# Kernel tuning notes

Measured on AMD Instinct MI355X. Metric: run time of the kernel, lower is better.

Reference implementation:

```python
import jax, jax.numpy as jnp
import numpy as np

N_NODES = 50000
N_EDGES = 800000
IN_CH = 64
OUT_CH = 64
HEADS = 4
NEG_SLOPE = 0.2  # PyG GATConv default


def setup_inputs() -> dict:
    key = jax.random.key(0)
    ks = jax.random.split(key, 8)
    x = jax.random.normal(ks[0], (N_NODES, IN_CH), dtype=jnp.float32)
    edge_index = jax.random.randint(ks[1], (2, N_EDGES), 0, N_NODES, dtype=jnp.int64)
    # GATConv params (concat=False): lin weight [in, H*out], att vectors [H, out], bias [out]
    W = jax.random.normal(ks[2], (IN_CH, HEADS * OUT_CH), dtype=jnp.float32) * (1.0 / np.sqrt(IN_CH))
    att_src = jax.random.normal(ks[3], (HEADS, OUT_CH), dtype=jnp.float32) * 0.1
    att_dst = jax.random.normal(ks[4], (HEADS, OUT_CH), dtype=jnp.float32) * 0.1
    bias = jnp.zeros((OUT_CH,), dtype=jnp.float32)
    fc_w = jax.random.normal(ks[5], (OUT_CH, 1), dtype=jnp.float32) * (1.0 / np.sqrt(OUT_CH))
    fc_b = jnp.zeros((1,), dtype=jnp.float32)
    return {"x": x, "edge_index": edge_index, "W": W, "att_src": att_src,
            "att_dst": att_dst, "bias": bias, "fc_w": fc_w, "fc_b": fc_b}


def reference(x, edge_index, W, att_src, att_dst, bias, fc_w, fc_b):
    N = x.shape[0]
    H, C = att_src.shape
    # per-node linear transform -> [N, H, C]
    xt = (x @ W).reshape(N, H, C)
    # PyG default add_self_loops=True
    loop = jnp.arange(N, dtype=edge_index.dtype)
    src = jnp.concatenate([edge_index[0], loop])  # message source j
    dst = jnp.concatenate([edge_index[1], loop])  # aggregation target i
    # attention logits: a_l . x_j + a_r . x_i, leaky_relu
    a_src = jnp.einsum('nhc,hc->nh', xt, att_src)  # [N, H]
    a_dst = jnp.einsum('nhc,hc->nh', xt, att_dst)
    e = jax.nn.leaky_relu(a_src[src] + a_dst[dst], NEG_SLOPE)  # [E, H]
    # segment softmax over incoming edges of each dst node
    m = jax.ops.segment_max(e, dst, num_segments=N)            # [N, H]
    e = jnp.exp(e - m[dst])
    s = jax.ops.segment_sum(e, dst, num_segments=N)            # [N, H]
    alpha = e / s[dst]                                          # [E, H]
    # weighted scatter-aggregate
    msg = xt[src] * alpha[:, :, None]                           # [E, H, C]
    out = jax.ops.segment_sum(msg, dst, num_segments=N)         # [N, H, C]
    out = out.mean(axis=1) + bias                               # concat=False -> mean heads
    h = jax.nn.relu(out)
    scores = (h @ fc_w + fc_b).squeeze(-1)                      # [N]
    return scores
```

## Files before the change

kernel.cpp:

```cpp
#include <hip/hip_runtime.h>
#include <hip/hip_bf16.h>

#define N_NODES 50000
#define N_EDGES 800000
#define HEADS   4
#define NEG_SLOPE 0.2f
#define CAP     64
#define NT      ((N_NODES + 63) / 64)
#define EPB     2048
#define NREG    196
#define QCAP    4608
#define INV_LN2 1.44269504088896340736f

typedef __attribute__((ext_vector_type(8))) _Float16 half8;
typedef __attribute__((ext_vector_type(4))) float f32x4;
typedef __attribute__((ext_vector_type(8))) unsigned short u16x8;

template <typename T> __device__ __forceinline__ float cvt(T v);
template <> __device__ __forceinline__ float cvt<float>(float v) { return v; }
template <> __device__ __forceinline__ float cvt<__hip_bfloat16>(__hip_bfloat16 v) {
    return __bfloat162float(v);
}
__device__ __forceinline__ unsigned short f2h(float f) {
    _Float16 h = (_Float16)f;
    return __builtin_bit_cast(unsigned short, h);
}
__device__ __forceinline__ float hbits(unsigned short u) {
    return (float)__builtin_bit_cast(_Float16, u);
}
__device__ __forceinline__ int probe_fp32(const unsigned* xw) {
    int sane = 0;
    for (int j = 0; j < 64; ++j) {
        unsigned e = (xw[j] >> 7) & 0xFF;
        sane += (e >= 90 && e <= 141);
    }
    return sane < 32;
}
__device__ __forceinline__ float loadW(int isf32, const void* W, int idx) {
    return isf32 ? ((const float*)W)[idx]
                 : cvt<__hip_bfloat16>(((const __hip_bfloat16*)W)[idx]);
}

template <typename T>
__device__ __forceinline__ void load8_f16(const T* p, _Float16* dst);
template <>
__device__ __forceinline__ void load8_f16<float>(const float* p, _Float16* dst) {
    float4 a = *(const float4*)p;
    float4 b = *(const float4*)(p + 4);
    dst[0] = (_Float16)a.x; dst[1] = (_Float16)a.y;
    dst[2] = (_Float16)a.z; dst[3] = (_Float16)a.w;
    dst[4] = (_Float16)b.x; dst[5] = (_Float16)b.y;
    dst[6] = (_Float16)b.z; dst[7] = (_Float16)b.w;
}
template <>
__device__ __forceinline__ void load8_f16<__hip_bfloat16>(const __hip_bfloat16* p,
                                                          _Float16* dst) {
    uint4 a = *(const uint4*)p;
    const unsigned short* u = (const unsigned short*)&a;
#pragma unroll
    for (int j = 0; j < 8; ++j)
        dst[j] = (_Float16)__uint_as_float(((unsigned)u[j]) << 16);
}

__global__ __launch_bounds__(256) void k_init(const unsigned* __restrict__ xw,
                                              const int* __restrict__ ei,
                                              const void* __restrict__ W,
                                              const void* __restrict__ att_src,
                                              const void* __restrict__ att_dst,
                                              int* __restrict__ qcnt,
                                              int* __restrict__ flags,
                                              unsigned short* __restrict__ Batt,
                                              unsigned short* __restrict__ Bpost) {
    __shared__ float waS[256], waD[256];
    __shared__ int f32sh;
    if (blockIdx.x == 0) {
        if (threadIdx.x < NREG) qcnt[threadIdx.x] = 0;
        if (threadIdx.x == 0) {
            int all0 = 1;
            for (int j = 1; j < 64; j += 2) all0 &= (ei[j] == 0);
            flags[0] = all0;
            flags[1] = probe_fp32(xw);
        }
        return;
    }
    const int pb = blockIdx.x - 1;
    if (threadIdx.x == 0) f32sh = probe_fp32(xw);
    __syncthreads();
    const int isf32 = f32sh;
    if (pb == 0) {
        int t = threadIdx.x, k = t >> 2, h = t & 3;
        float s = 0.f, d = 0.f;
        for (int c = 0; c < 64; ++c) {
            float w = loadW(isf32, W, k * 256 + h * 64 + c);
            float as = isf32 ? ((const float*)att_src)[h * 64 + c]
                             : cvt<__hip_bfloat16>(((const __hip_bfloat16*)att_src)[h * 64 + c]);
            float ad = isf32 ? ((const float*)att_dst)[h * 64 + c]
                             : cvt<__hip_bfloat16>(((const __hip_bfloat16*)att_dst)[h * 64 + c]);
            s = fmaf(w, as, s);
            d = fmaf(w, ad, d);
        }
        waS[t] = s * INV_LN2;
        waD[t] = d * INV_LN2;
        __syncthreads();
        if (threadIdx.x < 128) {
            int r = threadIdx.x;
            int q = (r >> 6) & 1, l = r & 63, n = l & 15;
            int kbase = q * 32 + ((l >> 4) & 3) * 8;
#pragma unroll
            for (int j = 0; j < 8; ++j) {
                int kk = kbase + j;
                float v = (n < 4) ? waS[kk * 4 + n]
                        : (n < 8) ? waD[kk * 4 + (n - 4)] : 0.f;
                Batt[r * 8 + j] = f2h(v);
            }
        }
    } else {
        const int sub = threadIdx.x >> 5, s = threadIdx.x & 31;
        const int t = (pb - 1) * 8 + sub;
        const int kt = t >> 2, nt = t & 3;
#pragma unroll
        for (int e = 0; e < 16; ++e) {
            int idx = s * 16 + e;
            int l = idx >> 3, j = idx & 7;
            int rs = kt * 32 + ((l >> 4) & 3) * 8 + j;
            int h = rs >> 6, k_in = rs & 63;
            int c = nt * 16 + (l & 15);
            Bpost[t * 512 + l * 8 + j] =
                f2h(loadW(isf32, W, k_in * 256 + h * 64 + c) * 0.25f);
        }
    }
}

template <typename T>
__device__ __forceinline__ void row_body(const T* __restrict__ x,
                                         const unsigned short* __restrict__ Batt,
                                         unsigned short* __restrict__ x16,
                                         float* __restrict__ a_src,
                                         float* __restrict__ a_dst) {
    const int tid = threadIdx.x;
    const int wav = tid >> 6, lane = tid & 63;
    const int quad = lane >> 4, r15 = lane & 15;
    const int m0 = blockIdx.x * 64;
    int gr = m0 + wav * 16 + r15;
    if (gr >= N_NODES) gr = N_NODES - 1;
    half8 afrag[2];
#pragma unroll
    for (int q = 0; q < 2; ++q) {
        _Float16 tmp[8];
        load8_f16<T>(x + (size_t)gr * 64 + q * 32 + quad * 8, tmp);
#pragma unroll
        for (int j = 0; j < 8; ++j) afrag[q][j] = tmp[j];
    }
    f32x4 acc = (f32x4){0.f, 0.f, 0.f, 0.f};
    const half8* bp = (const half8*)Batt;
    acc = __builtin_amdgcn_mfma_f32_16x16x32_f16(afrag[0], bp[lane], acc, 0, 0, 0);
    acc = __builtin_amdgcn_mfma_f32_16x16x32_f16(afrag[1], bp[64 + lane], acc, 0, 0, 0);
    if (r15 < 8) {
#pragma unroll
        for (int r = 0; r < 4; ++r) {
            int grow = m0 + wav * 16 + quad * 4 + r;
            if (grow < N_NODES) {
                if (r15 < 4) a_src[grow * HEADS + r15]       = acc[r];
                else         a_dst[grow * HEADS + (r15 - 4)] = acc[r];
            }
        }
    }
    {
        int row = m0 + (tid >> 2), seg = tid & 3;
        if (row < N_NODES) {
            _Float16 tmp[16];
            load8_f16<T>(x + (size_t)row * 64 + seg * 16, tmp);
            load8_f16<T>(x + (size_t)row * 64 + seg * 16 + 8, tmp + 8);
            *(u16x8*)(x16 + (size_t)row * 64 + seg * 16)     = *(const u16x8*)tmp;
            *(u16x8*)(x16 + (size_t)row * 64 + seg * 16 + 8) = *(const u16x8*)(tmp + 8);
        }
    }
}

__global__ __launch_bounds__(256) void k_mid(const void* __restrict__ x,
                                             const unsigned short* __restrict__ Batt,
                                             const int* __restrict__ ei,
                                             const int* __restrict__ flags,
                                             int* __restrict__ qcnt,
                                             unsigned* __restrict__ queue,
                                             unsigned short* __restrict__ x16,
                                             float* __restrict__ a_src,
                                             float* __restrict__ a_dst) {
    __shared__ int hist[NREG];
    __shared__ int qbaseS[NREG];
    const int tid = threadIdx.x;
    const bool edge_blk = ((blockIdx.x & 1) == 0);
    const int eb = blockIdx.x >> 1;
    unsigned rec[8]; int reg[8], lpos[8];
    int histv = 0, mybase = 0;
    if (edge_blk) {
        if (tid < NREG) hist[tid] = 0;
        __syncthreads();
        const int f64 = flags[0];
        const int pbase = eb * 1024 + tid;
#pragma unroll
        for (int k = 0; k < 4; ++k) {
            int pid = pbase + k * 256;
            int e = 2 * pid;
            if (e < N_EDGES) {
                int s0, d0, s1, d1;
                if (f64) {
                    int4 sv = *(const int4*)(ei + 2 * e);
                    int4 dv = *(const int4*)(ei + 2 * N_EDGES + 2 * e);
                    s0 = sv.x; s1 = sv.z; d0 = dv.x; d1 = dv.z;
                } else {
                    int2 sv = *(const int2*)(ei + e);
                    int2 dv = *(const int2*)(ei + N_EDGES + e);
                    s0 = sv.x; s1 = sv.y; d0 = dv.x; d1 = dv.y;
                }
                reg[2 * k]     = d0 >> 8;
                rec[2 * k]     = (unsigned)s0 | ((unsigned)d0 << 16);
                reg[2 * k + 1] = d1 >> 8;
                rec[2 * k + 1] = (unsigned)s1 | ((unsigned)d1 << 16);
            } else { reg[2 * k] = -1; reg[2 * k + 1] = -1; }
        }
#pragma unroll
        for (int k = 0; k < 8; ++k)
            if (reg[k] >= 0) lpos[k] = atomicAdd(&hist[reg[k]], 1);
        __syncthreads();
        if (tid < NREG) {
            histv = hist[tid];
            if (histv) mybase = atomicAdd(qcnt + tid, histv);
        }
    }
    if (flags[1]) row_body<float>((const float*)x, Batt, x16, a_src, a_dst);
    else          row_body<__hip_bfloat16>((const __hip_bfloat16*)x, Batt,
                                           x16, a_src, a_dst);
    if (edge_blk) {
        if (tid < NREG) qbaseS[tid] = mybase;
        __syncthreads();
#pragma unroll
        for (int k = 0; k < 8; ++k)
            if (reg[k] >= 0) {
                int o = qbaseS[reg[k]] + lpos[k];
                if (o < QCAP)
                    queue[(size_t)reg[k] * QCAP + o] = rec[k];
            }
    }
}

__global__ __launch_bounds__(256) void k_scat(const unsigned* __restrict__ queue,
                                              const int* __restrict__ qcnt,
                                              unsigned short* __restrict__ col_pad) {
    __shared__ int cl[256];
    const int b = blockIdx.x, tid = threadIdx.x;
    const int base = b << 8;
    cl[tid] = 0;
    __syncthreads();
    int m = qcnt[b]; m = m > QCAP ? QCAP : m;
    const unsigned* q = queue + (size_t)b * QCAP;
    for (int i = tid; i < m; i += 256) {
        unsigned rec = q[i];
        int d = rec >> 16, s = rec & 0xffff;
        int p = atomicAdd(&cl[d - base], 1);
        if (p < CAP - 1) col_pad[(size_t)d * CAP + p] = (unsigned short)s;
    }
    __syncthreads();
    int j = base + tid;
    if (j < N_NODES) {
        int c = cl[tid]; c = c > CAP - 1 ? CAP - 1 : c;
        col_pad[(size_t)j * CAP + (CAP - 1)] = (unsigned short)c;
    }
}

__global__ __launch_bounds__(256) void k_aggregate(const unsigned short* __restrict__ col_pad,
                                                   const float* __restrict__ a_src,
                                                   const float* __restrict__ a_dst,
                                                   const unsigned short* __restrict__ x16,
                                                   unsigned short* __restrict__ s_cat) {
    __shared__ __align__(16) int cS[4][64];
    __shared__ float4 peS[4][64];
    const int tid = threadIdx.x;
    const int wav = tid >> 6, lane = tid & 63;
    const int hlf = lane >> 5, l5 = lane & 31;
    const int wid = (blockIdx.x * blockDim.x + tid) >> 6;
    if (wid >= N_NODES) return;
    int* cSw = cS[wav];
    float4* peSw = peS[wav];
    const int cval = (int)col_pad[(size_t)wid * CAP + lane];
    const int n = __shfl(cval, 63, 64);
    const float4 ad = ((const float4*)a_dst)[wid];
    const int mycol = (lane < n) ? cval : wid;
    const float4 as = ((const float4*)a_src)[mycol];
    float e0 = as.x + ad.x, e1 = as.y + ad.y;
    float e2 = as.z + ad.z, e3 = as.w + ad.w;
    e0 = e0 > 0.f ? e0 : NEG_SLOPE * e0;  e1 = e1 > 0.f ? e1 : NEG_SLOPE * e1;
    e2 = e2 > 0.f ? e2 : NEG_SLOPE * e2;  e3 = e3 > 0.f ? e3 : NEG_SLOPE * e3;
    float4 pe = make_float4(exp2f(e0), exp2f(e1), exp2f(e2), exp2f(e3));
    if (lane > n) pe = make_float4(0.f, 0.f, 0.f, 0.f);
    const int slot = (lane & 1) * 32 + (lane >> 1);
    cSw[slot] = mycol << 7;
    peS[wav][slot] = pe;
    const char* xb = (const char*)x16 + l5 * 4;
    float a0 = 0.f, a1 = 0.f, a2 = 0.f, a3 = 0.f;
    float a4 = 0.f, a5 = 0.f, a6 = 0.f, a7 = 0.f;
    float sp0 = 0.f, sp1 = 0.f, sp2 = 0.f, sp3 = 0.f;
    const int nr = (n + 2) >> 1;
    const int*    cB = cSw + hlf * 32;
    const float4* pB = peSw + hlf * 32;
#define ACC2(D, P) { float x0 = hbits((unsigned short)((D) & 0xffff)); \
                     float x1 = hbits((unsigned short)((D) >> 16)); \
                     a0 = fmaf((P).x, x0, a0); a1 = fmaf((P).x, x1, a1); \
                     a2 = fmaf((P).y, x0, a2); a3 = fmaf((P).y, x1, a3); \
                     a4 = fmaf((P).z, x0, a4); a5 = fmaf((P).z, x1, a5); \
                     a6 = fmaf((P).w, x0, a6); a7 = fmaf((P).w, x1, a7); \
                     sp0 += (P).x; sp1 += (P).y; sp2 += (P).z; sp3 += (P).w; }
    int r = 0;
    for (; r + 4 <= nr; r += 4) {
        const int4 cc = *(const int4*)(cB + r);
        unsigned dA = *(const unsigned*)(xb + cc.x);
        unsigned dB = *(const unsigned*)(xb + cc.y);
        unsigned dC = *(const unsigned*)(xb + cc.z);
        unsigned dD = *(const unsigned*)(xb + cc.w);
        float4 pA = pB[r], pBv = pB[r + 1], pC = pB[r + 2], pD = pB[r + 3];
        ACC2(dA, pA); ACC2(dB, pBv); ACC2(dC, pC); ACC2(dD, pD);
    }
    for (; r < nr; ++r) {
        int c = cB[r];
        unsigned d = *(const unsigned*)(xb + c);
        float4 p = pB[r];
        ACC2(d, p);
    }
#undef ACC2
    a0 += __shfl_xor(a0, 32, 64); a1 += __shfl_xor(a1, 32, 64);
    a2 += __shfl_xor(a2, 32, 64); a3 += __shfl_xor(a3, 32, 64);
    a4 += __shfl_xor(a4, 32, 64); a5 += __shfl_xor(a5, 32, 64);
    a6 += __shfl_xor(a6, 32, 64); a7 += __shfl_xor(a7, 32, 64);
    sp0 += __shfl_xor(sp0, 32, 64); sp1 += __shfl_xor(sp1, 32, 64);
    sp2 += __shfl_xor(sp2, 32, 64); sp3 += __shfl_xor(sp3, 32, 64);
    const float r0 = 1.f / sp0, r1 = 1.f / sp1;
    const float r2 = 1.f / sp2, r3 = 1.f / sp3;
    unsigned short* sr = s_cat + (size_t)wid * 256 + 2 * l5;
    unsigned w0 = (unsigned)f2h(a0 * r0) | ((unsigned)f2h(a1 * r0) << 16);
    unsigned w1 = (unsigned)f2h(a2 * r1) | ((unsigned)f2h(a3 * r1) << 16);
    unsigned w2 = (unsigned)f2h(a4 * r2) | ((unsigned)f2h(a5 * r2) << 16);
    unsigned w3 = (unsigned)f2h(a6 * r3) | ((unsigned)f2h(a7 * r3) << 16);
    *(unsigned*)(sr)       = w0;
    *(unsigned*)(sr + 64)  = w1;
    *(unsigned*)(sr + 128) = w2;
    *(unsigned*)(sr + 192) = w3;
}

template <typename T>
__device__ __forceinline__ void post_body(const unsigned short* __restrict__ s_cat,
                                          const unsigned short* __restrict__ Bpost,
                                          const T* __restrict__ bias,
                                          const T* __restrict__ fc_w,
                                          const T* __restrict__ fc_b,
                                          float* __restrict__ out) {
    const int tid = threadIdx.x;
    const int wav = tid >> 6, lane = tid & 63;
    const int quad = lane >> 4, r15 = lane & 15;
    const int m0 = blockIdx.x * 64;
    int gr = m0 + wav * 16 + r15;
    if (gr >= N_NODES) gr = N_NODES - 1;
    const half8* arow = (const half8*)((const char*)s_cat + (size_t)gr * 512);
    half8 af[8];
#pragma unroll
    for (int kt = 0; kt < 8; ++kt) af[kt] = arow[kt * 4 + quad];
    f32x4 acc[4];
#pragma unroll
    for (int nt = 0; nt < 4; ++nt) acc[nt] = (f32x4){0.f, 0.f, 0.f, 0.f};
    const half8* bp = (const half8*)Bpost;
#pragma unroll
    for (int kt = 0; kt < 8; ++kt)
#pragma unroll
        for (int nt = 0; nt < 4; ++nt)
            acc[nt] = __builtin_amdgcn_mfma_f32_16x16x32_f16(
                af[kt], bp[(kt * 4 + nt) * 64 + lane], acc[nt], 0, 0, 0);
    float bi[4], fw[4];
#pragma unroll
    for (int nt = 0; nt < 4; ++nt) {
        int c = nt * 16 + r15;
        bi[nt] = cvt<T>(bias[c]);
        fw[nt] = cvt<T>(fc_w[c]);
    }
    const float fcb = cvt<T>(fc_b[0]);
#pragma unroll
    for (int r = 0; r < 4; ++r) {
        float p = 0.f;
#pragma unroll
        for (int nt = 0; nt < 4; ++nt) {
            float o = acc[nt][r] + bi[nt];
            o = o > 0.f ? o : 0.f;
            p = fmaf(o, fw[nt], p);
        }
#pragma unroll
        for (int off = 8; off > 0; off >>= 1) p += __shfl_xor(p, off, 64);
        int row = m0 + wav * 16 + quad * 4 + r;
        if (r15 == 0 && row < N_NODES) out[row] = p + fcb;
    }
}

__global__ __launch_bounds__(256) void k_post(const unsigned short* __restrict__ s_cat,
                                              const unsigned short* __restrict__ Bpost,
                                              const void* __restrict__ bias,
                                              const void* __restrict__ fc_w,
                                              const void* __restrict__ fc_b,
                                              const int* __restrict__ flags,
                                              float* __restrict__ out) {
    if (flags[1])
        post_body<float>(s_cat, Bpost, (const float*)bias, (const float*)fc_w,
                         (const float*)fc_b, out);
    else
        post_body<__hip_bfloat16>(s_cat, Bpost, (const __hip_bfloat16*)bias,
                                  (const __hip_bfloat16*)fc_w,
                                  (const __hip_bfloat16*)fc_b, out);
}

extern "C" void kernel_launch(void* const* d_in, const int* in_sizes, int n_in,
                              void* d_out, int out_size, void* d_ws, size_t ws_size,
                              hipStream_t stream) {
    const void* x       = d_in[0];
    const int*  ei      = (const int*)d_in[1];
    const void* W       = d_in[2];
    const void* att_src = d_in[3];
    const void* att_dst = d_in[4];
    const void* bias    = d_in[5];
    const void* fc_w    = d_in[6];
    const void* fc_b    = d_in[7];
    float* out = (float*)d_out;

    char* wsb = (char*)d_ws;
    unsigned short* x16   = (unsigned short*)wsb;
    unsigned short* s_cat = (unsigned short*)(wsb + 6400000);
    unsigned* queue = (unsigned*)s_cat;
    unsigned short* Batt  = (unsigned short*)(wsb + 32000000);
    unsigned short* Bpost = (unsigned short*)(wsb + 32002048);
    float* a_src = (float*)(wsb + 32034816);
    float* a_dst = (float*)(wsb + 32834816);
    unsigned short* col_pad = (unsigned short*)(wsb + 33634816);
    int* flags = (int*)(wsb + 40034816);
    int* qcnt  = (int*)(wsb + 40034824);

    k_init<<<6, 256, 0, stream>>>((const unsigned*)x, ei, W, att_src,
                                  att_dst, qcnt, flags, Batt, Bpost);
    k_mid<<<NT, 256, 0, stream>>>(x, Batt, ei, flags, qcnt, queue,
                                  x16, a_src, a_dst);
    k_scat<<<NREG, 256, 0, stream>>>(queue, qcnt, col_pad);
    k_aggregate<<<((size_t)N_NODES * 64 + 255) / 256, 256, 0, stream>>>(
        col_pad, a_src, a_dst, x16, s_cat);
    k_post<<<NT, 256, 0, stream>>>(s_cat, Bpost, bias, fc_w, fc_b, flags, out);
}
```

Baseline: 165.9 us.

## Fuse post-projection into aggregate kernel and halve dst bucket size

The post projection (MFMA over the aggregated heads, bias, relu, fc) now runs inside the aggregate kernel. It uses 1024-thread blocks of 16 nodes and keeps the per-node aggregate in shared memory, so the s_cat round trip through global memory and one kernel launch go away. Destination buckets shrink from 256 to 128 nodes, which doubles the region count and scatter blocks. The x16 fp16 copy is now written from the MFMA A-fragments instead of a second load of x. Risks are block-wide syncs in a large block and lower occupancy from the bigger shared memory footprint.

```diff
diff --git a/kernel.cpp b/kernel.cpp
--- a/kernel.cpp
+++ b/kernel.cpp
@@ -8,8 +8,10 @@
 #define CAP     64
 #define NT      ((N_NODES + 63) / 64)
 #define EPB     2048
-#define NREG    196
-#define QCAP    4608
+#define NCHUNK  ((N_EDGES + EPB - 1) / EPB)
+#define NREG    391
+#define QCAP    2560
+#define NAGG    (N_NODES / 16)
 #define INV_LN2 1.44269504088896340736f
 
 typedef __attribute__((ext_vector_type(8))) _Float16 half8;
@@ -74,7 +76,7 @@
     __shared__ float waS[256], waD[256];
     __shared__ int f32sh;
     if (blockIdx.x == 0) {
-        if (threadIdx.x < NREG) qcnt[threadIdx.x] = 0;
+        for (int t = threadIdx.x; t < NREG; t += 256) qcnt[t] = 0;
         if (threadIdx.x == 0) {
             int all0 = 1;
             for (int j = 1; j < 64; j += 2) all0 &= (ei[j] == 0);
@@ -141,7 +143,8 @@
     const int wav = tid >> 6, lane = tid & 63;
     const int quad = lane >> 4, r15 = lane & 15;
     const int m0 = blockIdx.x * 64;
-    int gr = m0 + wav * 16 + r15;
+    const int grow_a = m0 + wav * 16 + r15;
+    int gr = grow_a;
     if (gr >= N_NODES) gr = N_NODES - 1;
     half8 afrag[2];
 #pragma unroll
@@ -150,6 +153,11 @@
         load8_f16<T>(x + (size_t)gr * 64 + q * 32 + quad * 8, tmp);
 #pragma unroll
         for (int j = 0; j < 8; ++j) afrag[q][j] = tmp[j];
+    }
+    if (grow_a < N_NODES) {
+#pragma unroll
+        for (int q = 0; q < 2; ++q)
+            *(half8*)(x16 + (size_t)grow_a * 64 + q * 32 + quad * 8) = afrag[q];
     }
     f32x4 acc = (f32x4){0.f, 0.f, 0.f, 0.f};
     const half8* bp = (const half8*)Batt;
@@ -163,16 +171,6 @@
                 if (r15 < 4) a_src[grow * HEADS + r15]       = acc[r];
                 else         a_dst[grow * HEADS + (r15 - 4)] = acc[r];
             }
-        }
-    }
-    {
-        int row = m0 + (tid >> 2), seg = tid & 3;
-        if (row < N_NODES) {
-            _Float16 tmp[16];
-            load8_f16<T>(x + (size_t)row * 64 + seg * 16, tmp);
-            load8_f16<T>(x + (size_t)row * 64 + seg * 16 + 8, tmp + 8);
-            *(u16x8*)(x16 + (size_t)row * 64 + seg * 16)     = *(const u16x8*)tmp;
-            *(u16x8*)(x16 + (size_t)row * 64 + seg * 16 + 8) = *(const u16x8*)(tmp + 8);
         }
     }
 }
@@ -192,9 +190,9 @@
     const bool edge_blk = ((blockIdx.x & 1) == 0);
     const int eb = blockIdx.x >> 1;
     unsigned rec[8]; int reg[8], lpos[8];
-    int histv = 0, mybase = 0;
+    int histv0 = 0, histv1 = 0, mybase0 = 0, mybase1 = 0;
     if (edge_blk) {
-        if (tid < NREG) hist[tid] = 0;
+        for (int t = tid; t < NREG; t += 256) hist[t] = 0;
         __syncthreads();
         const int f64 = flags[0];
         const int pbase = eb * 1024 + tid;
@@ -213,9 +211,9 @@
                     int2 dv = *(const int2*)(ei + N_EDGES + e);
                     s0 = sv.x; s1 = sv.y; d0 = dv.x; d1 = dv.y;
                 }
-                reg[2 * k]     = d0 >> 8;
+                reg[2 * k]     = d0 >> 7;
                 rec[2 * k]     = (unsigned)s0 | ((unsigned)d0 << 16);
-                reg[2 * k + 1] = d1 >> 8;
+                reg[2 * k + 1] = d1 >> 7;
                 rec[2 * k + 1] = (unsigned)s1 | ((unsigned)d1 << 16);
             } else { reg[2 * k] = -1; reg[2 * k + 1] = -1; }
         }
@@ -223,16 +221,22 @@
         for (int k = 0; k < 8; ++k)
             if (reg[k] >= 0) lpos[k] = atomicAdd(&hist[reg[k]], 1);
         __syncthreads();
-        if (tid < NREG) {
-            histv = hist[tid];
-            if (histv) mybase = atomicAdd(qcnt + tid, histv);
+        {
+            int t0 = tid, t1 = tid + 256;
+            histv0 = hist[t0];
+            if (histv0) mybase0 = atomicAdd(qcnt + t0, histv0);
+            if (t1 < NREG) {
+                histv1 = hist[t1];
+                if (histv1) mybase1 = atomicAdd(qcnt + t1, histv1);
+            }
         }
     }
     if (flags[1]) row_body<float>((const float*)x, Batt, x16, a_src, a_dst);
     else          row_body<__hip_bfloat16>((const __hip_bfloat16*)x, Batt,
                                            x16, a_src, a_dst);
     if (edge_blk) {
-        if (tid < NREG) qbaseS[tid] = mybase;
+        qbaseS[tid] = mybase0;
+        if (tid + 256 < NREG) qbaseS[tid + 256] = mybase1;
         __syncthreads();
 #pragma unroll
         for (int k = 0; k < 8; ++k)
@@ -247,10 +251,10 @@
 __global__ __launch_bounds__(256) void k_scat(const unsigned* __restrict__ queue,
                                               const int* __restrict__ qcnt,
                                               unsigned short* __restrict__ col_pad) {
-    __shared__ int cl[256];
+    __shared__ int cl[128];
     const int b = blockIdx.x, tid = threadIdx.x;
-    const int base = b << 8;
-    cl[tid] = 0;
+    const int base = b << 7;
+    if (tid < 128) cl[tid] = 0;
     __syncthreads();
     int m = qcnt[b]; m = m > QCAP ? QCAP : m;
     const unsigned* q = queue + (size_t)b * QCAP;
@@ -261,27 +265,36 @@
         if (p < CAP - 1) col_pad[(size_t)d * CAP + p] = (unsigned short)s;
     }
     __syncthreads();
-    int j = base + tid;
-    if (j < N_NODES) {
-        int c = cl[tid]; c = c > CAP - 1 ? CAP - 1 : c;
-        col_pad[(size_t)j * CAP + (CAP - 1)] = (unsigned short)c;
-    }
-}
-
-__global__ __launch_bounds__(256) void k_aggregate(const unsigned short* __restrict__ col_pad,
-                                                   const float* __restrict__ a_src,
-                                                   const float* __restrict__ a_dst,
-                                                   const unsigned short* __restrict__ x16,
-                                                   unsigned short* __restrict__ s_cat) {
-    __shared__ __align__(16) int cS[4][64];
-    __shared__ float4 peS[4][64];
+    if (tid < 128) {
+        int j = base + tid;
+        if (j < N_NODES) {
+            int c = cl[tid]; c = c > CAP - 1 ? CAP - 1 : c;
+            col_pad[(size_t)j * CAP + (CAP - 1)] = (unsigned short)c;
+        }
+    }
+}
+
+template <typename T>
+__device__ __forceinline__ void agg_body(const unsigned short* __restrict__ col_pad,
+                                         const float* __restrict__ a_src,
+                                         const float* __restrict__ a_dst,
+                                         const unsigned short* __restrict__ x16,
+                                         const unsigned short* __restrict__ Bpost,
+                                         const T* __restrict__ bias,
+                                         const T* __restrict__ fc_w,
+                                         const T* __restrict__ fc_b,
+                                         float* __restrict__ out,
+                                         int* __restrict__ cS,
+                                         float4* __restrict__ peS,
+                                         unsigned* __restrict__ sS,
+                                         float* __restrict__ postS) {
     const int tid = threadIdx.x;
     const int wav = tid >> 6, lane = tid & 63;
     const int hlf = lane >> 5, l5 = lane & 31;
-    const int wid = (blockIdx.x * blockDim.x + tid) >> 6;
-    if (wid >= N_NODES) return;
-    int* cSw = cS[wav];
-    float4* peSw = peS[wav];
+    const int quad = lane >> 4, r15 = lane & 15;
+    const int wid = blockIdx.x * 16 + wav;
+    int* cSw = cS + wav * 64;
+    float4* peSw = peS + wav * 64;
     const int cval = (int)col_pad[(size_t)wid * CAP + lane];
     const int n = __shfl(cval, 63, 64);
     const float4 ad = ((const float4*)a_dst)[wid];
@@ -295,7 +308,7 @@
     if (lane > n) pe = make_float4(0.f, 0.f, 0.f, 0.f);
     const int slot = (lane & 1) * 32 + (lane >> 1);
     cSw[slot] = mycol << 7;
-    peS[wav][slot] = pe;
+    peSw[slot] = pe;
     const char* xb = (const char*)x16 + l5 * 4;
     float a0 = 0.f, a1 = 0.f, a2 = 0.f, a3 = 0.f;
     float a4 = 0.f, a5 = 0.f, a6 = 0.f, a7 = 0.f;
@@ -335,82 +348,69 @@
     sp2 += __shfl_xor(sp2, 32, 64); sp3 += __shfl_xor(sp3, 32, 64);
     const float r0 = 1.f / sp0, r1 = 1.f / sp1;
     const float r2 = 1.f / sp2, r3 = 1.f / sp3;
-    unsigned short* sr = s_cat + (size_t)wid * 256 + 2 * l5;
-    unsigned w0 = (unsigned)f2h(a0 * r0) | ((unsigned)f2h(a1 * r0) << 16);
-    unsigned w1 = (unsigned)f2h(a2 * r1) | ((unsigned)f2h(a3 * r1) << 16);
-    unsigned w2 = (unsigned)f2h(a4 * r2) | ((unsigned)f2h(a5 * r2) << 16);
-    unsigned w3 = (unsigned)f2h(a6 * r3) | ((unsigned)f2h(a7 * r3) << 16);
-    *(unsigned*)(sr)       = w0;
-    *(unsigned*)(sr + 64)  = w1;
-    *(unsigned*)(sr + 128) = w2;
-    *(unsigned*)(sr + 192) = w3;
-}
-
-template <typename T>
-__device__ __forceinline__ void post_body(const unsigned short* __restrict__ s_cat,
-                                          const unsigned short* __restrict__ Bpost,
-                                          const T* __restrict__ bias,
-                                          const T* __restrict__ fc_w,
-                                          const T* __restrict__ fc_b,
-                                          float* __restrict__ out) {
-    const int tid = threadIdx.x;
-    const int wav = tid >> 6, lane = tid & 63;
-    const int quad = lane >> 4, r15 = lane & 15;
-    const int m0 = blockIdx.x * 64;
-    int gr = m0 + wav * 16 + r15;
-    if (gr >= N_NODES) gr = N_NODES - 1;
-    const half8* arow = (const half8*)((const char*)s_cat + (size_t)gr * 512);
-    half8 af[8];
-#pragma unroll
-    for (int kt = 0; kt < 8; ++kt) af[kt] = arow[kt * 4 + quad];
-    f32x4 acc[4];
-#pragma unroll
-    for (int nt = 0; nt < 4; ++nt) acc[nt] = (f32x4){0.f, 0.f, 0.f, 0.f};
-    const half8* bp = (const half8*)Bpost;
-#pragma unroll
-    for (int kt = 0; kt < 8; ++kt)
-#pragma unroll
-        for (int nt = 0; nt < 4; ++nt)
-            acc[nt] = __builtin_amdgcn_mfma_f32_16x16x32_f16(
-                af[kt], bp[(kt * 4 + nt) * 64 + lane], acc[nt], 0, 0, 0);
-    float bi[4], fw[4];
-#pragma unroll
-    for (int nt = 0; nt < 4; ++nt) {
-        int c = nt * 16 + r15;
-        bi[nt] = cvt<T>(bias[c]);
-        fw[nt] = cvt<T>(fc_w[c]);
-    }
-    const float fcb = cvt<T>(fc_b[0]);
-#pragma unroll
-    for (int r = 0; r < 4; ++r) {
-        float p = 0.f;
-#pragma unroll
-        for (int nt = 0; nt < 4; ++nt) {
-            float o = acc[nt][r] + bi[nt];
+    if (lane < 32) {
+        unsigned* sr = sS + wav * 132;
+        sr[l5]      = (unsigned)f2h(a0 * r0) | ((unsigned)f2h(a1 * r0) << 16);
+        sr[32 + l5] = (unsigned)f2h(a2 * r1) | ((unsigned)f2h(a3 * r1) << 16);
+        sr[64 + l5] = (unsigned)f2h(a4 * r2) | ((unsigned)f2h(a5 * r2) << 16);
+        sr[96 + l5] = (unsigned)f2h(a6 * r3) | ((unsigned)f2h(a7 * r3) << 16);
+    }
+    __syncthreads();
+    if (wav < 4) {
+        const int nt = wav;
+        f32x4 acc = (f32x4){0.f, 0.f, 0.f, 0.f};
+        const half8* bp = (const half8*)Bpost;
+#pragma unroll
+        for (int kt = 0; kt < 8; ++kt) {
+            half8 af = *(const half8*)&sS[r15 * 132 + kt * 16 + quad * 4];
+            acc = __builtin_amdgcn_mfma_f32_16x16x32_f16(
+                af, bp[(kt * 4 + nt) * 64 + lane], acc, 0, 0, 0);
+        }
+        const float bi = cvt<T>(bias[nt * 16 + r15]);
+        const float fw = cvt<T>(fc_w[nt * 16 + r15]);
+#pragma unroll
+        for (int rr = 0; rr < 4; ++rr) {
+            float o = acc[rr] + bi;
             o = o > 0.f ? o : 0.f;
-            p = fmaf(o, fw[nt], p);
-        }
-#pragma unroll
-        for (int off = 8; off > 0; off >>= 1) p += __shfl_xor(p, off, 64);
-        int row = m0 + wav * 16 + quad * 4 + r;
-        if (r15 == 0 && row < N_NODES) out[row] = p + fcb;
-    }
-}
-
-__global__ __launch_bounds__(256) void k_post(const unsigned short* __restrict__ s_cat,
-                                              const unsigned short* __restrict__ Bpost,
-                                              const void* __restrict__ bias,
-                                              const void* __restrict__ fc_w,
-                                              const void* __restrict__ fc_b,
-                                              const int* __restrict__ flags,
-                                              float* __restrict__ out) {
+            float p = o * fw;
+            p += __shfl_xor(p, 1, 64); p += __shfl_xor(p, 2, 64);
+            p += __shfl_xor(p, 4, 64); p += __shfl_xor(p, 8, 64);
+            if (r15 == 0) postS[(quad * 4 + rr) * 4 + nt] = p;
+        }
+    }
+    __syncthreads();
+    if (tid < 16) {
+        float o = postS[tid * 4] + postS[tid * 4 + 1]
+                + postS[tid * 4 + 2] + postS[tid * 4 + 3] + cvt<T>(fc_b[0]);
+        out[blockIdx.x * 16 + tid] = o;
+    }
+}
+
+__global__ __launch_bounds__(1024, 4) void k_aggregate(
+        const unsigned short* __restrict__ col_pad,
+        const float* __restrict__ a_src,
+        const float* __restrict__ a_dst,
+        const unsigned short* __restrict__ x16,
+        const unsigned short* __restrict__ Bpost,
+        const void* __restrict__ bias,
+        const void* __restrict__ fc_w,
+        const void* __restrict__ fc_b,
+        const int* __restrict__ flags,
+        float* __restrict__ out) {
+    __shared__ __align__(16) int cS[16 * 64];
+    __shared__ float4 peS[16 * 64];
+    __shared__ __align__(16) unsigned sS[16 * 132];
+    __shared__ float postS[16 * 4];
     if (flags[1])
-        post_body<float>(s_cat, Bpost, (const float*)bias, (const float*)fc_w,
-                         (const float*)fc_b, out);
+        agg_body<float>(col_pad, a_src, a_dst, x16, Bpost, (const float*)bias,
+                        (const float*)fc_w, (const float*)fc_b, out,
+                        cS, peS, sS, postS);
     else
-        post_body<__hip_bfloat16>(s_cat, Bpost, (const __hip_bfloat16*)bias,
-                                  (const __hip_bfloat16*)fc_w,
-                                  (const __hip_bfloat16*)fc_b, out);
+        agg_body<__hip_bfloat16>(col_pad, a_src, a_dst, x16, Bpost,
+                                 (const __hip_bfloat16*)bias,
+                                 (const __hip_bfloat16*)fc_w,
+                                 (const __hip_bfloat16*)fc_b, out,
+                                 cS, peS, sS, postS);
 }
 
 extern "C" void kernel_launch(void* const* d_in, const int* in_sizes, int n_in,
@@ -428,22 +428,20 @@
 
     char* wsb = (char*)d_ws;
     unsigned short* x16   = (unsigned short*)wsb;
-    unsigned short* s_cat = (unsigned short*)(wsb + 6400000);
-    unsigned* queue = (unsigned*)s_cat;
-    unsigned short* Batt  = (unsigned short*)(wsb + 32000000);
-    unsigned short* Bpost = (unsigned short*)(wsb + 32002048);
-    float* a_src = (float*)(wsb + 32034816);
-    float* a_dst = (float*)(wsb + 32834816);
-    unsigned short* col_pad = (unsigned short*)(wsb + 33634816);
-    int* flags = (int*)(wsb + 40034816);
-    int* qcnt  = (int*)(wsb + 40034824);
+    unsigned*       queue = (unsigned*)(wsb + 6400000);
+    unsigned short* col_pad = (unsigned short*)(wsb + 10403840);
+    float* a_src = (float*)(wsb + 16803840);
+    float* a_dst = (float*)(wsb + 17603840);
+    unsigned short* Batt  = (unsigned short*)(wsb + 18403840);
+    unsigned short* Bpost = (unsigned short*)(wsb + 18405888);
+    int* flags = (int*)(wsb + 18438656);
+    int* qcnt  = (int*)(wsb + 18438664);
 
     k_init<<<6, 256, 0, stream>>>((const unsigned*)x, ei, W, att_src,
                                   att_dst, qcnt, flags, Batt, Bpost);
     k_mid<<<NT, 256, 0, stream>>>(x, Batt, ei, flags, qcnt, queue,
                                   x16, a_src, a_dst);
     k_scat<<<NREG, 256, 0, stream>>>(queue, qcnt, col_pad);
-    k_aggregate<<<((size_t)N_NODES * 64 + 255) / 256, 256, 0, stream>>>(
-        col_pad, a_src, a_dst, x16, s_cat);
-    k_post<<<NT, 256, 0, stream>>>(s_cat, Bpost, bias, fc_w, fc_b, flags, out);
-}
+    k_aggregate<<<NAGG, 1024, 0, stream>>>(col_pad, a_src, a_dst, x16, Bpost,
+                                           bias, fc_w, fc_b, flags, out);
+}
```

Result: slower. 178.9 us (+7.8%).
